# Kernel optimization log

Hardware: AMD Instinct MI355X
Metric: run time of the kernel (lower is better)

## Reference

```python
import jax, jax.numpy as jnp
import numpy as np

B, T, DM = 1, 8192, 1024
DS, DC, EXP = 16, 4, 2
DI = DM * EXP  # 2048


def setup_inputs() -> dict:
    key = jax.random.key(0)
    ks = jax.random.split(key, 6)
    sc = lambda k, shape, s: jax.random.normal(k, shape, jnp.float32) * s
    return {
        "x": jax.random.normal(ks[0], (B, T, DM), jnp.float32),
        "W_in": sc(ks[1], (DM, 2 * DI), 0.02),        # stored [in, out]
        "conv_w": sc(ks[2], (DI, 1, DC), 0.2),        # depthwise conv weight (OIH)
        "conv_b": jnp.zeros((DI,), jnp.float32),
        "W_x": sc(ks[3], (DI, 2 * DS + 1), 0.02),     # stored [in, out]
        "A_log": jnp.log(jnp.arange(1, DS + 1, dtype=jnp.float32)),
        "D": jnp.ones((DI,), jnp.float32),
        "W_out": sc(ks[4], (DI, DM), 0.02),           # stored [in, out]
    }


def reference(x, W_in, conv_w, conv_b, W_x, A_log, D, W_out):
    Bq, Tq, _ = x.shape
    # input projection and gate split
    xz = x @ W_in                              # [B,T,2*DI]
    xc, z = jnp.split(xz, 2, axis=-1)          # each [B,T,DI]
    # causal depthwise conv1d (pad left DC-1 == torch pad both + truncate [:T])
    xcT = jnp.transpose(xc, (0, 2, 1))         # [B,DI,T]
    conv = jax.lax.conv_general_dilated(
        xcT, conv_w, window_strides=(1,), padding=[(DC - 1, 0)],
        feature_group_count=DI)
    conv = conv + conv_b[None, :, None]
    xs = jax.nn.silu(jnp.transpose(conv, (0, 2, 1)))   # [B,T,DI]
    # selective SSM parameters (single shared delta per timestep)
    x_dbl = xs @ W_x                           # [B,T,2N+1]
    delta = jax.nn.softplus(x_dbl[..., :1])    # [B,T,1]
    Bp = x_dbl[..., 1:1 + DS]                  # [B,T,N]
    Cp = x_dbl[..., 1 + DS:]                   # [B,T,N]
    A = -jnp.exp(A_log)                        # [N]
    A_bar = jnp.exp(delta * A)                 # [B,T,N]
    B_bar = delta * Bp                         # [B,T,N]

    def step(h, inp):
        a_t, b_t, x_t, c_t = inp               # [B,N],[B,N],[B,DI],[B,N]
        h = a_t[:, None, :] * h + b_t[:, None, :] * x_t[:, :, None]  # [B,DI,N]
        y_t = jnp.einsum('bdn,bn->bd', h, c_t)
        return h, y_t

    h0 = jnp.zeros((Bq, DI, DS), xs.dtype)
    seq = (jnp.swapaxes(A_bar, 0, 1), jnp.swapaxes(B_bar, 0, 1),
           jnp.swapaxes(xs, 0, 1), jnp.swapaxes(Cp, 0, 1))
    _, ys = jax.lax.scan(step, h0, seq)        # ys: [T,B,DI]
    y = jnp.swapaxes(ys, 0, 1) + D * xs        # [B,T,DI]
    y = y * jax.nn.silu(z)
    return y @ W_out                           # [B,T,DM]
```

## Files before the change

### kernel.cpp

```cpp
#include <hip/hip_runtime.h>
#include <hip/hip_bf16.h>

#define T_SEQ 8192
#define DMODEL 1024
#define DINNER 2048
#define NSTATE 16
#define NCH 128
#define CL 64

typedef __attribute__((ext_vector_type(8))) short bf16x8;
typedef __attribute__((ext_vector_type(4))) float f32x4;

__device__ __forceinline__ float bf2f(ushort u) {
  union { unsigned u; float f; } c; c.u = ((unsigned)u) << 16; return c.f;
}
__device__ __forceinline__ ushort f2bf(float f) {
  union { float f; unsigned u; } c; c.f = f;
  unsigned r = c.u + 0x7FFFu + ((c.u >> 16) & 1u);
  return (ushort)(r >> 16);
}

#define GLD16(dst, src) __builtin_amdgcn_global_load_lds( \
    (const __attribute__((address_space(1))) void*)(src), \
    (__attribute__((address_space(3))) void*)(dst), 16, 0, 0)

template<int N> __device__ __forceinline__ void waitcnt_vm() {
  asm volatile("s_waitcnt vmcnt(%0)" :: "i"(N) : "memory");
}
#define LGKM0() do { asm volatile("s_waitcnt lgkmcnt(0)" ::: "memory"); \
                     __builtin_amdgcn_sched_barrier(0); } while (0)
#define BAR() do { __builtin_amdgcn_s_barrier(); \
                   __builtin_amdgcn_sched_barrier(0); } while (0)

__global__ __launch_bounds__(256) void prep_all(const float* __restrict__ x,
                                                const float* __restrict__ W_in,
                                                const float* __restrict__ W_out,
                                                const float* __restrict__ Wx,
                                                ushort* __restrict__ xbf,
                                                ushort* __restrict__ winT,
                                                ushort* __restrict__ woutT,
                                                ushort* __restrict__ wxT) {
  __shared__ float tile[32][33];
  int b = blockIdx.x, tid = threadIdx.x;
  if (b < 8192) {
    int i = b * 256 + tid;
    float4 v = ((const float4*)x)[i];
    ushort4 o;
    o.x = f2bf(v.x); o.y = f2bf(v.y); o.z = f2bf(v.z); o.w = f2bf(v.w);
    ((ushort4*)xbf)[i] = o;
    return;
  }
  b -= 8192;
  const float* in; ushort* out; int R, C, bx, by;
  if (b < 4096)      { in = W_in;  out = winT;  R = 1024; C = 4096; bx = b & 127; by = b >> 7; }
  else if (b < 6144) { b -= 4096; in = W_out; out = woutT; R = 2048; C = 1024; bx = b & 31; by = b >> 5; }
  else {
    int idx = (b - 6144) * 256 + tid;
    int j = idx >> 11, k = idx & 2047;
    wxT[idx] = (j < 33) ? f2bf(Wx[k * 33 + j]) : (ushort)0;
    return;
  }
  int xx = tid & 31, yy = tid >> 5;
  bx *= 32; by *= 32;
#pragma unroll
  for (int j = 0; j < 32; j += 8)
    tile[yy + j][xx] = in[(size_t)(by + yy + j) * C + bx + xx];
  __syncthreads();
#pragma unroll
  for (int j = 0; j < 32; j += 8)
    out[(size_t)(bx + yy + j) * R + by + xx] = f2bf(tile[xx][yy + j]);
}

template<int OUTMODE, int MR>
__global__ __launch_bounds__(512, 2)
void gemm8p(const ushort* __restrict__ A, const ushort* __restrict__ B,
            void* __restrict__ out0, void* __restrict__ out1,
            int N, int K, int LDK, int MX) {
  constexpr int BM = MR * 32;
  constexpr int H = MR / 2;
  constexpr int AHL = BM / 128;
  constexpr int VM = 2 * AHL + 2;
  extern __shared__ __align__(16) char smem[];
  char* const sBr = smem + 2 * BM * 128;

  const int tid = threadIdx.x, lane = tid & 63, wid = tid >> 6;
  const int wm = wid >> 2, wn = wid & 3;
  const int xcd = blockIdx.x & 7, jb = blockIdx.x >> 3;
  const int mtile = xcd * MX + (jb % MX), ntile = jb / MX;
  const int mbase = mtile * BM, nbase = ntile * 256;
  const int NT = K >> 6;

  const int sr = tid >> 3;
  const int scol = ((tid & 7) ^ (sr & 7)) << 3;
  const ushort* pA = A + (size_t)(mbase + sr) * LDK + scol;
  const ushort* pB = B + (size_t)(nbase + sr) * LDK + scol;

  auto stgA = [&](int buf, int h, int tt) {
#pragma unroll
    for (int r = 0; r < AHL; ++r)
      GLD16(smem + buf * (BM * 128) + (h * (BM / 2) + r * 64) * 128 + wid * 1024,
            pA + (size_t)(h * (BM / 2) + r * 64) * LDK + (size_t)tt * 64);
  };
  auto stgB = [&](int buf, int h, int tt) {
#pragma unroll
    for (int r = 0; r < 2; ++r)
      GLD16(sBr + buf * 32768 + (h * 128 + r * 64) * 128 + wid * 1024,
            pB + (size_t)(h * 128 + r * 64) * LDK + (size_t)tt * 64);
  };

  const int frow = lane & 15, hh = lane >> 4;
  const int sw[2] = { ((hh) ^ (frow & 7)) << 4, ((4 + hh) ^ (frow & 7)) << 4 };
  const int arow = (wm * (MR * 16) + frow) * 128;
  const int brow = (wn * 64 + frow) * 128;

  f32x4 acc[MR][4];
#pragma unroll
  for (int m = 0; m < MR; ++m)
#pragma unroll
    for (int n = 0; n < 4; ++n) acc[m][n] = (f32x4){0.f, 0.f, 0.f, 0.f};

  stgA(0, 0, 0); stgA(0, 1, 0); stgB(0, 0, 0); stgB(0, 1, 0);
  if (NT > 1) { stgA(1, 0, 1); stgA(1, 1, 1); stgB(1, 0, 1); }
  waitcnt_vm<VM>();
  BAR();

  for (int t = 0; t < NT; ++t) {
    const int b = t & 1;
    const char* bA = smem + b * (BM * 128);
    const char* bB = sBr + b * 32768;
    bf16x8 alo[H][2], ahi[H][2], b01[2][2], b23[2][2];

#pragma unroll
    for (int m = 0; m < H; ++m)
#pragma unroll
      for (int kk = 0; kk < 2; ++kk)
        alo[m][kk] = *(const bf16x8*)(bA + arow + m * 2048 + sw[kk]);
#pragma unroll
    for (int n = 0; n < 2; ++n)
#pragma unroll
      for (int kk = 0; kk < 2; ++kk)
        b01[n][kk] = *(const bf16x8*)(bB + brow + n * 2048 + sw[kk]);
    if (t + 1 < NT) stgB((t + 1) & 1, 1, t + 1);
    BAR(); LGKM0();
    __builtin_amdgcn_s_setprio(1);
#pragma unroll
    for (int kk = 0; kk < 2; ++kk)
#pragma unroll
      for (int m = 0; m < H; ++m)
#pragma unroll
        for (int n = 0; n < 2; ++n)
          acc[m][n] = __builtin_amdgcn_mfma_f32_16x16x32_bf16(alo[m][kk], b01[n][kk], acc[m][n], 0, 0, 0);
    __builtin_amdgcn_s_setprio(0);
    BAR();

#pragma unroll
    for (int m = 0; m < H; ++m)
#pragma unroll
      for (int kk = 0; kk < 2; ++kk)
        ahi[m][kk] = *(const bf16x8*)(bA + arow + (H + m) * 2048 + sw[kk]);
    BAR(); LGKM0();
    __builtin_amdgcn_s_setprio(1);
#pragma unroll
    for (int kk = 0; kk < 2; ++kk)
#pragma unroll
      for (int m = 0; m < H; ++m)
#pragma unroll
        for (int n = 0; n < 2; ++n)
          acc[H + m][n] = __builtin_amdgcn_mfma_f32_16x16x32_bf16(ahi[m][kk], b01[n][kk], acc[H + m][n], 0, 0, 0);
    __builtin_amdgcn_s_setprio(0);
    BAR();

#pragma unroll
    for (int n = 0; n < 2; ++n)
#pragma unroll
      for (int kk = 0; kk < 2; ++kk)
        b23[n][kk] = *(const bf16x8*)(bB + brow + (2 + n) * 2048 + sw[kk]);
    if (t + 2 < NT) stgA(b, 0, t + 2);
    BAR(); LGKM0();
    __builtin_amdgcn_s_setprio(1);
#pragma unroll
    for (int kk = 0; kk < 2; ++kk)
#pragma unroll
      for (int m = 0; m < H; ++m)
#pragma unroll
        for (int n = 0; n < 2; ++n)
          acc[H + m][2 + n] = __builtin_amdgcn_mfma_f32_16x16x32_bf16(ahi[m][kk], b23[n][kk], acc[H + m][2 + n], 0, 0, 0);
    __builtin_amdgcn_s_setprio(0);
    BAR();

    if (t + 2 < NT) { stgA(b, 1, t + 2); stgB(b, 0, t + 2); }
    __builtin_amdgcn_s_setprio(1);
#pragma unroll
    for (int kk = 0; kk < 2; ++kk)
#pragma unroll
      for (int m = 0; m < H; ++m)
#pragma unroll
        for (int n = 0; n < 2; ++n)
          acc[m][2 + n] = __builtin_amdgcn_mfma_f32_16x16x32_bf16(alo[m][kk], b23[n][kk], acc[m][2 + n], 0, 0, 0);
    __builtin_amdgcn_s_setprio(0);
    if (t + 2 < NT) waitcnt_vm<VM>(); else waitcnt_vm<0>();
    BAR();
  }

  const int crow0 = mbase + wm * (MR * 16) + (lane >> 4) * 4;
  const int ccol0 = wn * 64 + (lane & 15);
  if (OUTMODE == 0) {
    float* po = (float*)out0;
#pragma unroll
    for (int m = 0; m < MR; ++m)
#pragma unroll
      for (int n = 0; n < 4; ++n)
#pragma unroll
        for (int j = 0; j < 4; ++j)
          po[(size_t)(crow0 + m * 16 + j) * N + nbase + ccol0 + n * 16] = acc[m][n][j];
  } else {
    ushort* dst = (nbase < 2048) ? (ushort*)out0 : (ushort*)out1;
    const int cbase = (nbase & 2047) + ccol0;
#pragma unroll
    for (int m = 0; m < MR; ++m)
#pragma unroll
      for (int n = 0; n < 4; ++n)
#pragma unroll
        for (int j = 0; j < 4; ++j)
          dst[(size_t)(crow0 + m * 16 + j) * 2048 + cbase + n * 16] = f2bf(acc[m][n][j]);
  }
}

__global__ __launch_bounds__(256) void gemm_thin(const ushort* __restrict__ A,
                                                 const ushort* __restrict__ Bw,
                                                 float* __restrict__ part) {
  __shared__ __align__(16) ushort sA[128 * 64];
  __shared__ __align__(16) ushort sB[48 * 64];
  const int tid = threadIdx.x, lane = tid & 63, wid = tid >> 6;
  const int mbase = blockIdx.x * 128;
  const int kbase = blockIdx.y * 512;
  const int frow = lane & 15, fke = (lane >> 4) * 8;

  f32x4 acc[2][3];
#pragma unroll
  for (int m = 0; m < 2; ++m)
#pragma unroll
    for (int n = 0; n < 3; ++n) acc[m][n] = (f32x4){0.f, 0.f, 0.f, 0.f};

  for (int k0 = 0; k0 < 512; k0 += 64) {
#pragma unroll
    for (int j = 0; j < 4; ++j) {
      int o = tid * 16 + j * 4096;
      int row = o >> 7, ke = ((o >> 4) & 7) * 8;
      GLD16((char*)sA + wid * 1024 + j * 4096,
            A + (size_t)(mbase + row) * DINNER + kbase + k0 + ke);
    }
    for (int i = tid; i < 384; i += 256) {
      int brow = i >> 3, kc = (i & 7) * 8;
      *(bf16x8*)&sB[brow * 64 + kc] = *(const bf16x8*)(Bw + (size_t)brow * DINNER + kbase + k0 + kc);
    }
    __syncthreads();
    bf16x8 af[2][2], bf_[3][2];
#pragma unroll
    for (int m = 0; m < 2; ++m)
#pragma unroll
      for (int ks = 0; ks < 2; ++ks)
        af[m][ks] = *(const bf16x8*)&sA[(wid * 32 + m * 16 + frow) * 64 + ks * 32 + fke];
#pragma unroll
    for (int n = 0; n < 3; ++n)
#pragma unroll
      for (int ks = 0; ks < 2; ++ks)
        bf_[n][ks] = *(const bf16x8*)&sB[(n * 16 + frow) * 64 + ks * 32 + fke];
#pragma unroll
    for (int ks = 0; ks < 2; ++ks)
#pragma unroll
      for (int m = 0; m < 2; ++m)
#pragma unroll
        for (int n = 0; n < 3; ++n)
          acc[m][n] = __builtin_amdgcn_mfma_f32_16x16x32_bf16(af[m][ks], bf_[n][ks], acc[m][n], 0, 0, 0);
    __syncthreads();
  }
  float* po = part + (size_t)blockIdx.y * (T_SEQ * 48);
#pragma unroll
  for (int m = 0; m < 2; ++m)
#pragma unroll
    for (int n = 0; n < 3; ++n)
#pragma unroll
      for (int j = 0; j < 4; ++j) {
        int rr = mbase + wid * 32 + m * 16 + (lane >> 4) * 4 + j;
        int cc = n * 16 + (lane & 15);
        po[(size_t)rr * 48 + cc] = acc[m][n][j];
      }
}

__global__ __launch_bounds__(256) void conv_silu(const ushort* __restrict__ xc,
                                                 const float* __restrict__ cw,
                                                 const float* __restrict__ cb,
                                                 ushort* __restrict__ xs) {
  int idx = blockIdx.x * 256 + threadIdx.x;
  int t = idx >> 11, d = idx & 2047;
  float4 w = *(const float4*)(cw + d * 4);
  float a = cb[d];
  const float wk[4] = {w.x, w.y, w.z, w.w};
#pragma unroll
  for (int k = 0; k < 4; ++k) {
    int tt = t - 3 + k;
    if (tt >= 0) a += bf2f(xc[(size_t)tt * 2048 + d]) * wk[k];
  }
  float s = a / (1.f + expf(-a));
  xs[idx] = f2bf(s);
}

__global__ __launch_bounds__(256) void precompute_k(const float* __restrict__ part,
                                                    const float* __restrict__ A_log,
                                                    float* __restrict__ abar,
                                                    float* __restrict__ bbar,
                                                    float* __restrict__ cc,
                                                    float* __restrict__ P) {
  __shared__ float ld[256 * 33];
  const int t0 = blockIdx.x * 256, tid = threadIdx.x;
  for (int i = tid; i < 256 * 33; i += 256) {
    int r = i / 33, col = i - r * 33;
    size_t off = (size_t)(t0 + r) * 48 + col;
    ld[i] = part[off] + part[(size_t)T_SEQ * 48 + off] +
            part[2 * (size_t)T_SEQ * 48 + off] + part[3 * (size_t)T_SEQ * 48 + off];
  }
  __syncthreads();
  const float* r = &ld[tid * 33];
  float v = r[0];
  float delta = (v > 20.f) ? v : log1pf(expf(v));
  int t = t0 + tid;
#pragma unroll
  for (int n = 0; n < NSTATE; ++n) {
    float A = -expf(A_log[n]);
    abar[t * 16 + n] = expf(delta * A);
    bbar[t * 16 + n] = delta * r[1 + n];
    cc[t * 16 + n]   = r[17 + n];
  }
  float s = delta;
#pragma unroll
  for (int off = 32; off > 0; off >>= 1) s += __shfl_down(s, off);
  s = __shfl(s, 0);
  int lane = tid & 63, c = blockIdx.x * 4 + (tid >> 6);
  if (lane < 16) P[c * 16 + lane] = expf(-expf(A_log[lane]) * s);
}

__global__ __launch_bounds__(256) void scan1(const ushort* __restrict__ xs,
                                             const float* __restrict__ abar,
                                             const float* __restrict__ bbar,
                                             ushort* __restrict__ hend) {
  int c = blockIdx.x;
  int d = blockIdx.y * 256 + threadIdx.x;
  __shared__ float s_ab[CL * 16], s_bb[CL * 16];
  for (int e = threadIdx.x; e < CL * 16; e += 256) {
    s_ab[e] = abar[(size_t)c * CL * 16 + e];
    s_bb[e] = bbar[(size_t)c * CL * 16 + e];
  }
  __syncthreads();
  float h[16];
#pragma unroll
  for (int n = 0; n < 16; ++n) h[n] = 0.f;
  int tbase = c * CL;
  for (int i = 0; i < CL; ++i) {
    float x = bf2f(xs[(size_t)(tbase + i) * DINNER + d]);
#pragma unroll
    for (int n = 0; n < 16; ++n) h[n] = s_ab[i * 16 + n] * h[n] + s_bb[i * 16 + n] * x;
  }
  ushort* o = hend + ((size_t)c * DINNER + d) * 16;
  bf16x8 o0, o1;
#pragma unroll
  for (int q = 0; q < 8; ++q) { o0[q] = (short)f2bf(h[q]); o1[q] = (short)f2bf(h[8 + q]); }
  *(bf16x8*)o = o0;
  *(bf16x8*)(o + 8) = o1;
}

__global__ __launch_bounds__(128) void scan2(const ushort* __restrict__ hend,
                                             const float* __restrict__ P,
                                             ushort* __restrict__ hin) {
  int idx = blockIdx.x * 128 + threadIdx.x;
  int n = idx & 15;
  float h = 0.f;
  for (int g = 0; g < 16; ++g) {
    float e[8], p[8];
#pragma unroll
    for (int j = 0; j < 8; ++j) {
      e[j] = bf2f(hend[(size_t)(g * 8 + j) * 32768 + idx]);
      p[j] = P[(g * 8 + j) * 16 + n];
    }
#pragma unroll
    for (int j = 0; j < 8; ++j) {
      hin[(size_t)(g * 8 + j) * 32768 + idx] = f2bf(h);
      h = p[j] * h + e[j];
    }
  }
}

__global__ __launch_bounds__(256) void scan3(const ushort* __restrict__ xs,
                                             const ushort* __restrict__ zb,
                                             const float* __restrict__ abar,
                                             const float* __restrict__ bbar,
                                             const float* __restrict__ cc,
                                             const ushort* __restrict__ hin,
                                             const float* __restrict__ Dv,
                                             ushort* __restrict__ y) {
  int c = blockIdx.x;
  int d = blockIdx.y * 256 + threadIdx.x;
  __shared__ float s_ab[CL * 16], s_bb[CL * 16], s_cc[CL * 16];
  for (int e = threadIdx.x; e < CL * 16; e += 256) {
    s_ab[e] = abar[(size_t)c * CL * 16 + e];
    s_bb[e] = bbar[(size_t)c * CL * 16 + e];
    s_cc[e] = cc[(size_t)c * CL * 16 + e];
  }
  __syncthreads();
  float h[16];
  const ushort* hi = hin + ((size_t)c * DINNER + d) * 16;
  bf16x8 h0 = *(const bf16x8*)hi, h1 = *(const bf16x8*)(hi + 8);
#pragma unroll
  for (int q = 0; q < 8; ++q) { h[q] = bf2f((ushort)h0[q]); h[8 + q] = bf2f((ushort)h1[q]); }
  float Dd = Dv[d];
  int tbase = c * CL;
  for (int i = 0; i < CL; ++i) {
    size_t t = tbase + i;
    float x = bf2f(xs[t * DINNER + d]);
    float ys = 0.f;
#pragma unroll
    for (int n = 0; n < 16; ++n) {
      h[n] = s_ab[i * 16 + n] * h[n] + s_bb[i * 16 + n] * x;
      ys += s_cc[i * 16 + n] * h[n];
    }
    float z = bf2f(zb[t * 2048 + d]);
    float yv = (ys + Dd * x) * (z / (1.f + expf(-z)));
    y[t * DINNER + d] = f2bf(yv);
  }
}

extern "C" void kernel_launch(void* const* d_in, const int* in_sizes, int n_in,
                              void* d_out, int out_size, void* d_ws, size_t ws_size,
                              hipStream_t stream) {
  const float* x      = (const float*)d_in[0];
  const float* W_in   = (const float*)d_in[1];
  const float* conv_w = (const float*)d_in[2];
  const float* conv_b = (const float*)d_in[3];
  const float* W_x    = (const float*)d_in[4];
  const float* A_log  = (const float*)d_in[5];
  const float* Dv     = (const float*)d_in[6];
  const float* W_out  = (const float*)d_in[7];
  float* out = (float*)d_out;

  char* w = (char*)d_ws;
  auto alloc = [&](size_t bytes) { char* p = w; w += (bytes + 255) & ~(size_t)255; return p; };

  ushort* xbf   = (ushort*)alloc((size_t)T_SEQ * DMODEL * 2);
  ushort* winT  = (ushort*)alloc((size_t)4096 * 1024 * 2);
  ushort* woutT = (ushort*)alloc((size_t)1024 * 2048 * 2);
  ushort* wxT   = (ushort*)alloc((size_t)48 * 2048 * 2);
  ushort* xc    = (ushort*)alloc((size_t)T_SEQ * DINNER * 2);
  ushort* zb    = (ushort*)alloc((size_t)T_SEQ * DINNER * 2);
  ushort* xs    = (ushort*)alloc((size_t)T_SEQ * DINNER * 2);
  float*  parts = (float*) alloc((size_t)4 * T_SEQ * 48 * 4);
  float*  abar  = (float*) alloc((size_t)T_SEQ * 16 * 4);
  float*  bbar  = (float*) alloc((size_t)T_SEQ * 16 * 4);
  float*  ccb   = (float*) alloc((size_t)T_SEQ * 16 * 4);
  float*  P     = (float*) alloc((size_t)NCH * 16 * 4);
  ushort* hend  = (ushort*)alloc((size_t)NCH * DINNER * 16 * 2);
  ushort* hin   = (ushort*)alloc((size_t)NCH * DINNER * 16 * 2);
  ushort* ybf   = (ushort*)alloc((size_t)T_SEQ * DINNER * 2);

  auto kg1 = gemm8p<1, 8>;
  auto kg3 = gemm8p<0, 4>;
  hipFuncSetAttribute(reinterpret_cast<const void*>(kg1),
                      hipFuncAttributeMaxDynamicSharedMemorySize, 131072);
  hipFuncSetAttribute(reinterpret_cast<const void*>(kg3),
                      hipFuncAttributeMaxDynamicSharedMemorySize, 98304);

  prep_all<<<dim3(14720), 256, 0, stream>>>(x, W_in, W_out, W_x, xbf, winT, woutT, wxT);

  kg1<<<dim3(512), 512, 131072, stream>>>(xbf, winT, xc, zb, 4096, 1024, 1024, 4);

  conv_silu<<<(T_SEQ * DINNER) / 256, 256, 0, stream>>>(xc, conv_w, conv_b, xs);

  gemm_thin<<<dim3(T_SEQ / 128, 4), 256, 0, stream>>>(xs, wxT, parts);

  precompute_k<<<32, 256, 0, stream>>>(parts, A_log, abar, bbar, ccb, P);

  scan1<<<dim3(NCH, DINNER / 256), 256, 0, stream>>>(xs, abar, bbar, hend);
  scan2<<<256, 128, 0, stream>>>(hend, P, hin);
  scan3<<<dim3(NCH, DINNER / 256), 256, 0, stream>>>(xs, zb, abar, bbar, ccb, hin, Dv, ybf);

  kg3<<<dim3(256), 512, 98304, stream>>>(ybf, woutT, out, nullptr, 1024, 2048, 2048, 8);
}
```

Before: 285.2 us.

## Replace 8-phase interleaved GEMM pipeline with simple two-barrier double-buffered loop

Replaces the eight-phase GEMM schedule with a simpler loop that loads all A and B fragments into registers, waits once, issues the next full tile prefetch, and runs all MFMAs in one block. Each K-step drops from about eight barriers to two, which cuts synchronisation overhead and simplifies the schedule. The cost is less fine-grained overlap of LDS reads and global loads with MFMA work, and more fragment registers held live at once, which could hurt occupancy at two blocks per CU.

```diff
diff --git a/kernel.cpp b/kernel.cpp
--- a/kernel.cpp
+++ b/kernel.cpp
@@ -27,10 +27,6 @@
 template<int N> __device__ __forceinline__ void waitcnt_vm() {
   asm volatile("s_waitcnt vmcnt(%0)" :: "i"(N) : "memory");
 }
-#define LGKM0() do { asm volatile("s_waitcnt lgkmcnt(0)" ::: "memory"); \
-                     __builtin_amdgcn_sched_barrier(0); } while (0)
-#define BAR() do { __builtin_amdgcn_s_barrier(); \
-                   __builtin_amdgcn_sched_barrier(0); } while (0)
 
 __global__ __launch_bounds__(256) void prep_all(const float* __restrict__ x,
                                                 const float* __restrict__ W_in,
@@ -73,13 +69,12 @@
 
 template<int OUTMODE, int MR>
 __global__ __launch_bounds__(512, 2)
-void gemm8p(const ushort* __restrict__ A, const ushort* __restrict__ B,
-            void* __restrict__ out0, void* __restrict__ out1,
-            int N, int K, int LDK, int MX) {
+void gemm_min(const ushort* __restrict__ A, const ushort* __restrict__ B,
+              void* __restrict__ out0, void* __restrict__ out1,
+              int N, int K, int LDK, int MX) {
   constexpr int BM = MR * 32;
-  constexpr int H = MR / 2;
   constexpr int AHL = BM / 128;
-  constexpr int VM = 2 * AHL + 2;
+  constexpr int S = (BM + 256) / 64;
   extern __shared__ __align__(16) char smem[];
   char* const sBr = smem + 2 * BM * 128;
 
@@ -95,17 +90,19 @@
   const ushort* pA = A + (size_t)(mbase + sr) * LDK + scol;
   const ushort* pB = B + (size_t)(nbase + sr) * LDK + scol;
 
-  auto stgA = [&](int buf, int h, int tt) {
-#pragma unroll
-    for (int r = 0; r < AHL; ++r)
-      GLD16(smem + buf * (BM * 128) + (h * (BM / 2) + r * 64) * 128 + wid * 1024,
-            pA + (size_t)(h * (BM / 2) + r * 64) * LDK + (size_t)tt * 64);
-  };
-  auto stgB = [&](int buf, int h, int tt) {
-#pragma unroll
-    for (int r = 0; r < 2; ++r)
-      GLD16(sBr + buf * 32768 + (h * 128 + r * 64) * 128 + wid * 1024,
-            pB + (size_t)(h * 128 + r * 64) * LDK + (size_t)tt * 64);
+  auto stage = [&](int buf, int tt) {
+#pragma unroll
+    for (int h = 0; h < 2; ++h)
+#pragma unroll
+      for (int r = 0; r < AHL; ++r)
+        GLD16(smem + buf * (BM * 128) + (h * (BM / 2) + r * 64) * 128 + wid * 1024,
+              pA + (size_t)(h * (BM / 2) + r * 64) * LDK + (size_t)tt * 64);
+#pragma unroll
+    for (int h = 0; h < 2; ++h)
+#pragma unroll
+      for (int r = 0; r < 2; ++r)
+        GLD16(sBr + buf * 32768 + (h * 128 + r * 64) * 128 + wid * 1024,
+              pB + (size_t)(h * 128 + r * 64) * LDK + (size_t)tt * 64);
   };
 
   const int frow = lane & 15, hh = lane >> 4;
@@ -119,87 +116,48 @@
 #pragma unroll
     for (int n = 0; n < 4; ++n) acc[m][n] = (f32x4){0.f, 0.f, 0.f, 0.f};
 
-  stgA(0, 0, 0); stgA(0, 1, 0); stgB(0, 0, 0); stgB(0, 1, 0);
-  if (NT > 1) { stgA(1, 0, 1); stgA(1, 1, 1); stgB(1, 0, 1); }
-  waitcnt_vm<VM>();
-  BAR();
+  stage(0, 0);
+  if (NT > 1) stage(1, 1);
+  waitcnt_vm<S>();
+  __builtin_amdgcn_s_barrier();
+  __builtin_amdgcn_sched_barrier(0);
 
   for (int t = 0; t < NT; ++t) {
     const int b = t & 1;
     const char* bA = smem + b * (BM * 128);
     const char* bB = sBr + b * 32768;
-    bf16x8 alo[H][2], ahi[H][2], b01[2][2], b23[2][2];
-
-#pragma unroll
-    for (int m = 0; m < H; ++m)
+
+    bf16x8 af[MR][2], bv[4][2];
+#pragma unroll
+    for (int m = 0; m < MR; ++m)
 #pragma unroll
       for (int kk = 0; kk < 2; ++kk)
-        alo[m][kk] = *(const bf16x8*)(bA + arow + m * 2048 + sw[kk]);
-#pragma unroll
-    for (int n = 0; n < 2; ++n)
+        af[m][kk] = *(const bf16x8*)(bA + arow + m * 2048 + sw[kk]);
+#pragma unroll
+    for (int n = 0; n < 4; ++n)
 #pragma unroll
       for (int kk = 0; kk < 2; ++kk)
-        b01[n][kk] = *(const bf16x8*)(bB + brow + n * 2048 + sw[kk]);
-    if (t + 1 < NT) stgB((t + 1) & 1, 1, t + 1);
-    BAR(); LGKM0();
+        bv[n][kk] = *(const bf16x8*)(bB + brow + n * 2048 + sw[kk]);
+
+    asm volatile("s_waitcnt lgkmcnt(0)" ::: "memory");
+    __builtin_amdgcn_s_barrier();
+    __builtin_amdgcn_sched_barrier(0);
+
+    if (t + 2 < NT) stage(b, t + 2);
+
     __builtin_amdgcn_s_setprio(1);
 #pragma unroll
     for (int kk = 0; kk < 2; ++kk)
 #pragma unroll
-      for (int m = 0; m < H; ++m)
-#pragma unroll
-        for (int n = 0; n < 2; ++n)
-          acc[m][n] = __builtin_amdgcn_mfma_f32_16x16x32_bf16(alo[m][kk], b01[n][kk], acc[m][n], 0, 0, 0);
+      for (int m = 0; m < MR; ++m)
+#pragma unroll
+        for (int n = 0; n < 4; ++n)
+          acc[m][n] = __builtin_amdgcn_mfma_f32_16x16x32_bf16(af[m][kk], bv[n][kk], acc[m][n], 0, 0, 0);
     __builtin_amdgcn_s_setprio(0);
-    BAR();
-
-#pragma unroll
-    for (int m = 0; m < H; ++m)
-#pragma unroll
-      for (int kk = 0; kk < 2; ++kk)
-        ahi[m][kk] = *(const bf16x8*)(bA + arow + (H + m) * 2048 + sw[kk]);
-    BAR(); LGKM0();
-    __builtin_amdgcn_s_setprio(1);
-#pragma unroll
-    for (int kk = 0; kk < 2; ++kk)
-#pragma unroll
-      for (int m = 0; m < H; ++m)
-#pragma unroll
-        for (int n = 0; n < 2; ++n)
-          acc[H + m][n] = __builtin_amdgcn_mfma_f32_16x16x32_bf16(ahi[m][kk], b01[n][kk], acc[H + m][n], 0, 0, 0);
-    __builtin_amdgcn_s_setprio(0);
-    BAR();
-
-#pragma unroll
-    for (int n = 0; n < 2; ++n)
-#pragma unroll
-      for (int kk = 0; kk < 2; ++kk)
-        b23[n][kk] = *(const bf16x8*)(bB + brow + (2 + n) * 2048 + sw[kk]);
-    if (t + 2 < NT) stgA(b, 0, t + 2);
-    BAR(); LGKM0();
-    __builtin_amdgcn_s_setprio(1);
-#pragma unroll
-    for (int kk = 0; kk < 2; ++kk)
-#pragma unroll
-      for (int m = 0; m < H; ++m)
-#pragma unroll
-        for (int n = 0; n < 2; ++n)
-          acc[H + m][2 + n] = __builtin_amdgcn_mfma_f32_16x16x32_bf16(ahi[m][kk], b23[n][kk], acc[H + m][2 + n], 0, 0, 0);
-    __builtin_amdgcn_s_setprio(0);
-    BAR();
-
-    if (t + 2 < NT) { stgA(b, 1, t + 2); stgB(b, 0, t + 2); }
-    __builtin_amdgcn_s_setprio(1);
-#pragma unroll
-    for (int kk = 0; kk < 2; ++kk)
-#pragma unroll
-      for (int m = 0; m < H; ++m)
-#pragma unroll
-        for (int n = 0; n < 2; ++n)
-          acc[m][2 + n] = __builtin_amdgcn_mfma_f32_16x16x32_bf16(alo[m][kk], b23[n][kk], acc[m][2 + n], 0, 0, 0);
-    __builtin_amdgcn_s_setprio(0);
-    if (t + 2 < NT) waitcnt_vm<VM>(); else waitcnt_vm<0>();
-    BAR();
+
+    if (t + 2 < NT) waitcnt_vm<S>(); else waitcnt_vm<0>();
+    __builtin_amdgcn_s_barrier();
+    __builtin_amdgcn_sched_barrier(0);
   }
 
   const int crow0 = mbase + wm * (MR * 16) + (lane >> 4) * 4;
@@ -461,8 +419,8 @@
   ushort* hin   = (ushort*)alloc((size_t)NCH * DINNER * 16 * 2);
   ushort* ybf   = (ushort*)alloc((size_t)T_SEQ * DINNER * 2);
 
-  auto kg1 = gemm8p<1, 8>;
-  auto kg3 = gemm8p<0, 4>;
+  auto kg1 = gemm_min<1, 8>;
+  auto kg3 = gemm_min<0, 4>;
   hipFuncSetAttribute(reinterpret_cast<const void*>(kg1),
                       hipFuncAttributeMaxDynamicSharedMemorySize, 131072);
   hipFuncSetAttribute(reinterpret_cast<const void*>(kg3),
```

Result: no change. 290.7 us (+1.9%).

## Add triple-buffered 256x128 GEMM kernel for output projection

Applied to the files above, without the earlier changes.

Adds a new GEMM kernel, gemm_nf, that uses 256x128 output tiles and a three-stage LDS ring fed by global_load_lds. It keeps two K-tiles in flight while computing on the third, raises MFMA priority with setprio, and uses XOR-swizzled LDS reads. The final W_out projection now uses this kernel instead of gemm8p<0,4>, with a different XCD-aware tile mapping (MX=4). It needs more shared memory (144 KB), which can limit occupancy, and the new tile shape changes how wave fragments are loaded.

```diff
diff --git a/kernel.cpp b/kernel.cpp
--- a/kernel.cpp
+++ b/kernel.cpp
@@ -226,6 +226,114 @@
   }
 }
 
+template<int OUTMODE>
+__global__ __launch_bounds__(512, 2)
+void gemm_nf(const ushort* __restrict__ A, const ushort* __restrict__ B,
+             void* __restrict__ out0, void* __restrict__ out1,
+             int N, int K, int LDK, int MX) {
+  extern __shared__ __align__(16) char smem[];
+  char* const sBr = smem + 98304;
+
+  const int tid = threadIdx.x, lane = tid & 63, wid = tid >> 6;
+  const int wm = wid >> 1, wn = wid & 1;
+  const int xcd = blockIdx.x & 7, jb = blockIdx.x >> 3;
+  const int mtile = xcd * MX + (jb % MX), ntile = jb / MX;
+  const int mbase = mtile * 256, nbase = ntile * 128;
+  const int NT = K >> 6;
+
+  const int sr = tid >> 3;
+  const int scol = ((tid & 7) ^ (sr & 7)) << 3;
+  const ushort* pA = A + (size_t)(mbase + sr) * LDK + scol;
+  const ushort* pB = B + (size_t)(nbase + sr) * LDK + scol;
+
+  auto stage = [&](int buf, int tt) {
+#pragma unroll
+    for (int j = 0; j < 4; ++j)
+      GLD16(smem + buf * 32768 + j * 8192 + wid * 1024,
+            pA + (size_t)(j * 64) * LDK + (size_t)tt * 64);
+#pragma unroll
+    for (int j = 0; j < 2; ++j)
+      GLD16(sBr + buf * 16384 + j * 8192 + wid * 1024,
+            pB + (size_t)(j * 64) * LDK + (size_t)tt * 64);
+  };
+
+  const int frow = lane & 15, hh = lane >> 4;
+  const int sw[2] = { ((hh) ^ (frow & 7)) << 4, ((4 + hh) ^ (frow & 7)) << 4 };
+  const int arow = (wm * 64 + frow) * 128;
+  const int brow = (wn * 64 + frow) * 128;
+
+  f32x4 acc[4][4];
+#pragma unroll
+  for (int m = 0; m < 4; ++m)
+#pragma unroll
+    for (int n = 0; n < 4; ++n) acc[m][n] = (f32x4){0.f, 0.f, 0.f, 0.f};
+
+  stage(0, 0);
+  if (NT > 1) stage(1, 1);
+  waitcnt_vm<6>();
+  __builtin_amdgcn_s_barrier();
+
+  int b = 0;
+  for (int t = 0; t < NT; ++t) {
+    if (t + 2 < NT) {
+      int b2 = b + 2; if (b2 >= 3) b2 -= 3;
+      stage(b2, t + 2);
+    }
+    const char* bA = smem + b * 32768;
+    const char* bB = sBr + b * 16384;
+
+    bf16x8 af[4][2], bv[4][2];
+#pragma unroll
+    for (int m = 0; m < 4; ++m)
+#pragma unroll
+      for (int kk = 0; kk < 2; ++kk)
+        af[m][kk] = *(const bf16x8*)(bA + arow + m * 2048 + sw[kk]);
+#pragma unroll
+    for (int n = 0; n < 4; ++n)
+#pragma unroll
+      for (int kk = 0; kk < 2; ++kk)
+        bv[n][kk] = *(const bf16x8*)(bB + brow + n * 2048 + sw[kk]);
+
+    __builtin_amdgcn_s_setprio(1);
+#pragma unroll
+    for (int kk = 0; kk < 2; ++kk)
+#pragma unroll
+      for (int m = 0; m < 4; ++m)
+#pragma unroll
+        for (int n = 0; n < 4; ++n)
+          acc[m][n] = __builtin_amdgcn_mfma_f32_16x16x32_bf16(af[m][kk], bv[n][kk], acc[m][n], 0, 0, 0);
+    __builtin_amdgcn_s_setprio(0);
+
+    asm volatile("s_waitcnt lgkmcnt(0)" ::: "memory");
+    if (t + 2 < NT) waitcnt_vm<6>(); else waitcnt_vm<0>();
+    __builtin_amdgcn_s_barrier();
+    b = (b == 2) ? 0 : b + 1;
+  }
+
+  const int crow0 = mbase + wm * 64 + (lane >> 4) * 4;
+  const int ccol0 = nbase + wn * 64 + (lane & 15);
+  if (OUTMODE == 0) {
+    float* po = (float*)out0;
+#pragma unroll
+    for (int m = 0; m < 4; ++m)
+#pragma unroll
+      for (int n = 0; n < 4; ++n)
+#pragma unroll
+        for (int j = 0; j < 4; ++j)
+          po[(size_t)(crow0 + m * 16 + j) * N + ccol0 + n * 16] = acc[m][n][j];
+  } else {
+    ushort* dst = (nbase < 2048) ? (ushort*)out0 : (ushort*)out1;
+    const int cbase = (nbase & 2047) + wn * 64 + (lane & 15);
+#pragma unroll
+    for (int m = 0; m < 4; ++m)
+#pragma unroll
+      for (int n = 0; n < 4; ++n)
+#pragma unroll
+        for (int j = 0; j < 4; ++j)
+          dst[(size_t)(crow0 + m * 16 + j) * 2048 + cbase + n * 16] = f2bf(acc[m][n][j]);
+  }
+}
+
 __global__ __launch_bounds__(256) void gemm_thin(const ushort* __restrict__ A,
                                                  const ushort* __restrict__ Bw,
                                                  float* __restrict__ part) {
@@ -462,11 +570,11 @@
   ushort* ybf   = (ushort*)alloc((size_t)T_SEQ * DINNER * 2);
 
   auto kg1 = gemm8p<1, 8>;
-  auto kg3 = gemm8p<0, 4>;
+  auto kg3 = gemm_nf<0>;
   hipFuncSetAttribute(reinterpret_cast<const void*>(kg1),
                       hipFuncAttributeMaxDynamicSharedMemorySize, 131072);
   hipFuncSetAttribute(reinterpret_cast<const void*>(kg3),
-                      hipFuncAttributeMaxDynamicSharedMemorySize, 98304);
+                      hipFuncAttributeMaxDynamicSharedMemorySize, 147456);
 
   prep_all<<<dim3(14720), 256, 0, stream>>>(x, W_in, W_out, W_x, xbf, winT, woutT, wxT);
 
@@ -482,5 +590,5 @@
   scan2<<<256, 128, 0, stream>>>(hend, P, hin);
   scan3<<<dim3(NCH, DINNER / 256), 256, 0, stream>>>(xs, zb, abar, bbar, ccb, hin, Dv, ybf);
 
-  kg3<<<dim3(256), 512, 98304, stream>>>(ybf, woutT, out, nullptr, 1024, 2048, 2048, 8);
-}
+  kg3<<<dim3(256), 512, 147456, stream>>>(ybf, woutT, out, nullptr, 1024, 2048, 2048, 4);
+}
```

After: 283.9 us. About the same (-0.4%).
